# Kernel tuning notes

Measured on AMD Instinct MI355X. Metric: run time of the kernel, lower is better.

The kernel has to match this reference:

```python
import jax, jax.numpy as jnp
import numpy as np

WS = (4, 4, 4)  # window size
HEADS = 3
HEAD_DIM = 32

def _relative_indices():
    idx = np.array([[x, y, z] for x in range(WS[0]) for y in range(WS[1]) for z in range(WS[2])])
    rel = idx[None, :, :] - idx[:, None, :]  # [T, T, 3]
    rel = rel - rel.min()
    return rel  # values in [0, 2*ws-2]

_REL = _relative_indices()

def setup_inputs() -> dict:
    key = jax.random.key(0)
    k1, k2, k3, k4, k5 = jax.random.split(key, 5)
    dim = 96
    inner = HEADS * HEAD_DIM  # 96
    x = jax.random.normal(k1, (2, 64, 64, 64, dim), dtype=jnp.float32)
    w_qkv = jax.random.normal(k2, (dim, inner * 3), dtype=jnp.float32) * 0.02
    pos_embedding = jax.random.normal(k3, (7, 7, 7), dtype=jnp.float32)
    w_out = jax.random.normal(k4, (inner, dim), dtype=jnp.float32) * 0.02
    b_out = jax.random.normal(k5, (dim,), dtype=jnp.float32) * 0.02
    return {"x": x, "w_qkv": w_qkv, "pos_embedding": pos_embedding,
            "w_out": w_out, "b_out": b_out}

def reference(x, w_qkv, pos_embedding, w_out, b_out):
    b, H, W, D, C = x.shape
    wh, ww, wd = WS
    nwh, nww, nwd = H // wh, W // ww, D // wd
    nw = nwh * nww * nwd
    T = wh * ww * wd  # tokens per window
    scale = HEAD_DIM ** -0.5

    qkv = x @ w_qkv  # [b,H,W,D,3*inner]
    q, k, v = jnp.split(qkv, 3, axis=-1)

    def to_windows(t):
        # [b,H,W,D,h*d] -> [b, h, nw, T, d]
        t = t.reshape(b, nwh, wh, nww, ww, nwd, wd, HEADS, HEAD_DIM)
        t = t.transpose(0, 7, 1, 3, 5, 2, 4, 6, 8)
        return t.reshape(b, HEADS, nw, T, HEAD_DIM)

    q, k, v = map(to_windows, (q, k, v))

    dots = jnp.einsum('bhwid,bhwjd->bhwij', q, k) * scale  # [b,h,nw,T,T]
    bias = pos_embedding[_REL[:, :, 0], _REL[:, :, 1], _REL[:, :, 2]]  # [T,T]
    attn = jax.nn.softmax(dots + bias, axis=-1)
    out = jnp.einsum('bhwij,bhwjd->bhwid', attn, v)  # [b,h,nw,T,d]

    # back to [b,H,W,D,h*d]
    out = out.reshape(b, HEADS, nwh, nww, nwd, wh, ww, wd, HEAD_DIM)
    out = out.transpose(0, 2, 5, 3, 6, 4, 7, 1, 8)
    out = out.reshape(b, H, W, D, HEADS * HEAD_DIM)
    return out @ w_out + b_out
```

## Files before the change

kernel.cpp:

```cpp
#include <hip/hip_runtime.h>


typedef __attribute__((ext_vector_type(8))) short bv8;
typedef __attribute__((ext_vector_type(4))) float fv4;

__device__ __forceinline__ unsigned short f2bf(float f) {
    union { float f; unsigned u; } v; v.f = f;
    unsigned r = v.u + 0x7fffu + ((v.u >> 16) & 1u);
    return (unsigned short)(r >> 16);
}

__device__ __forceinline__ unsigned pack2(float lo, float hi) {
    return (unsigned)f2bf(lo) | ((unsigned)f2bf(hi) << 16);
}

__device__ __forceinline__ bv8 cvt8(const float* __restrict__ p) {
    float4 a = *(const float4*)p;
    float4 b = *(const float4*)(p + 4);
    bv8 r;
    r[0] = (short)f2bf(a.x); r[1] = (short)f2bf(a.y);
    r[2] = (short)f2bf(a.z); r[3] = (short)f2bf(a.w);
    r[4] = (short)f2bf(b.x); r[5] = (short)f2bf(b.y);
    r[6] = (short)f2bf(b.z); r[7] = (short)f2bf(b.w);
    return r;
}

#define REBUILD(dst, lo, hi)  do {                                              \
    unsigned w0 = (unsigned)__shfl((int)(lo)[0], lsrc0, 64);                    \
    unsigned w1 = (unsigned)__shfl((int)(lo)[1], lsrc0, 64);                    \
    unsigned w2 = (unsigned)__shfl((int)(lo)[0], lsrc1, 64);                    \
    unsigned w3 = (unsigned)__shfl((int)(lo)[1], lsrc1, 64);                    \
    unsigned v0 = (unsigned)__shfl((int)(hi)[0], lsrc0, 64);                    \
    unsigned v1 = (unsigned)__shfl((int)(hi)[1], lsrc0, 64);                    \
    unsigned v2 = (unsigned)__shfl((int)(hi)[0], lsrc1, 64);                    \
    unsigned v3 = (unsigned)__shfl((int)(hi)[1], lsrc1, 64);                    \
    unsigned u0 = selhi ? v0 : w0, u1 = selhi ? v1 : w1;                        \
    unsigned u2 = selhi ? v2 : w2, u3 = selhi ? v3 : w3;                        \
    bv8 p_;                                                                     \
    p_[0] = (short)(u0 & 0xffffu); p_[1] = (short)(u0 >> 16);                   \
    p_[2] = (short)(u1 & 0xffffu); p_[3] = (short)(u1 >> 16);                   \
    p_[4] = (short)(u2 & 0xffffu); p_[5] = (short)(u2 >> 16);                   \
    p_[6] = (short)(u3 & 0xffffu); p_[7] = (short)(u3 >> 16);                   \
    dst = p_;                                                                   \
} while (0)

__global__ void prep_kernel(const float* __restrict__ wqkv,
                            const float* __restrict__ wout,
                            const float* __restrict__ pos,
                            float* __restrict__ biasT,
                            unsigned short* __restrict__ wqT,
                            unsigned short* __restrict__ woT)
{
    int id = blockIdx.x * 256 + threadIdx.x;
    if (id < 27648) {
        int n = id / 96, k = id % 96;
        wqT[id] = f2bf(wqkv[k * 288 + n]);
    } else if (id < 36864) {
        int j = id - 27648;
        int n = j / 96, k = j % 96;
        woT[j] = f2bf(wout[k * 96 + n]);
    } else {
        int i = id - 36864;
        int kj = i >> 6, qi = i & 63;
        int dh = ((kj >> 4) & 3) - ((qi >> 4) & 3) + 3;
        int dw = ((kj >> 2) & 3) - ((qi >> 2) & 3) + 3;
        int dd = (kj & 3) - (qi & 3) + 3;
        biasT[kj * 64 + qi] = pos[(dh * 7 + dw) * 7 + dd] * 1.4426950408889634f;
    }
}

__global__ void __launch_bounds__(256, 4) winattn_kernel(
    const float* __restrict__ x,
    const float* __restrict__ b_out,
    const float* __restrict__ biasT,
    const unsigned short* __restrict__ wqT,
    const unsigned short* __restrict__ woT,
    float* __restrict__ out)
{
    __shared__ __align__(16) unsigned short ks[64 * 104];
    __shared__ __align__(16) unsigned short vts[96 * 72];

    const int tid = threadIdx.x;
    const int w = tid >> 6, lane = tid & 63;
    const int c = lane & 15, g = lane >> 4;
    const int widx = blockIdx.x, bb = blockIdx.y;
    const int bh = (widx >> 8) & 15, bw2 = (widx >> 4) & 15, bd = widx & 15;

    const int ST_W = 64 * 96, ST_H = 64 * 64 * 96;
    const int xbase = ((bb * 64 + bh * 4) * 64 + bw2 * 4) * 64 * 96 + bd * 4 * 96;
    const int i0 = w * 16;

    const int lsrc0 = (((2 * g) & 3) << 4) + c;
    const int lsrc1 = (((2 * g + 1) & 3) << 4) + c;
    const bool selhi = (g & 2) != 0;

    bv8 af[3];
    {
        int t = i0 + c;
        const float* tp = x + xbase + (t >> 4) * ST_H + ((t >> 2) & 3) * ST_W + (t & 3) * 96;
#pragma unroll
        for (int k = 0; k < 3; ++k)
            af[k] = cvt8(tp + k * 32 + g * 8);
    }

    const unsigned short* bsrc = wqT + c * 96 + g * 8;
    bv8 b0[3], bn[3];
#pragma unroll
    for (int k = 0; k < 3; ++k) b0[k] = *(const bv8*)(bsrc + k * 32);

    unsigned pkq[6][2];
#pragma unroll
    for (int nt = 0; nt < 18; ++nt) {
        if (nt < 17) {
#pragma unroll
            for (int k = 0; k < 3; ++k) bn[k] = *(const bv8*)(bsrc + (nt + 1) * 1536 + k * 32);
        }
        fv4 acc = {0.f, 0.f, 0.f, 0.f};
        if (nt < 6) {
#pragma unroll
            for (int k = 0; k < 3; ++k)
                acc = __builtin_amdgcn_mfma_f32_16x16x32_bf16(b0[k], af[k], acc, 0, 0, 0);
            pkq[nt][0] = pack2(acc[0], acc[1]);
            pkq[nt][1] = pack2(acc[2], acc[3]);
        } else if (nt < 12) {
#pragma unroll
            for (int k = 0; k < 3; ++k)
                acc = __builtin_amdgcn_mfma_f32_16x16x32_bf16(af[k], b0[k], acc, 0, 0, 0);
#pragma unroll
            for (int r = 0; r < 4; ++r)
                ks[(i0 + 4 * g + r) * 104 + (nt - 6) * 16 + c] = f2bf(acc[r]);
        } else {
#pragma unroll
            for (int k = 0; k < 3; ++k)
                acc = __builtin_amdgcn_mfma_f32_16x16x32_bf16(af[k], b0[k], acc, 0, 0, 0);
            int d = (nt - 12) * 16 + c;
            *(unsigned*)&vts[d * 72 + i0 + 4 * g]     = pack2(acc[0], acc[1]);
            *(unsigned*)&vts[d * 72 + i0 + 4 * g + 2] = pack2(acc[2], acc[3]);
        }
#pragma unroll
        for (int k = 0; k < 3; ++k) b0[k] = bn[k];
    }

    bv8 qf[3];
#pragma unroll
    for (int h = 0; h < 3; ++h)
        REBUILD(qf[h], pkq[2 * h], pkq[2 * h + 1]);

    float brow[4][4];
#pragma unroll
    for (int nt = 0; nt < 4; ++nt)
#pragma unroll
        for (int r = 0; r < 4; ++r)
            brow[nt][r] = biasT[(nt * 16 + 4 * g + r) * 64 + i0 + c];

    __syncthreads();

    const float scale2 = 0.17677669529663687f * 1.4426950408889634f;
    unsigned pko[6][2];

#pragma unroll
    for (int h = 0; h < 3; ++h) {
        bv8 kf[4];
#pragma unroll
        for (int nt = 0; nt < 4; ++nt)
            kf[nt] = *(const bv8*)&ks[(nt * 16 + c) * 104 + h * 32 + g * 8];
        float sv[4][4];
#pragma unroll
        for (int nt = 0; nt < 4; ++nt) {
            fv4 z = {0.f, 0.f, 0.f, 0.f};
            fv4 s = __builtin_amdgcn_mfma_f32_16x16x32_bf16(kf[nt], qf[h], z, 0, 0, 0);
#pragma unroll
            for (int r = 0; r < 4; ++r)
                sv[nt][r] = s[r] * scale2 + brow[nt][r];
        }
        float sm = 0.f;
#pragma unroll
        for (int nt = 0; nt < 4; ++nt)
#pragma unroll
            for (int r = 0; r < 4; ++r) {
                float e = exp2f(sv[nt][r]);
                sv[nt][r] = e;
                sm += e;
            }
        sm += __shfl_xor(sm, 16, 64);
        sm += __shfl_xor(sm, 32, 64);
        float inv = __builtin_amdgcn_rcpf(sm);

        unsigned pk[4][2];
#pragma unroll
        for (int nt = 0; nt < 4; ++nt) {
            pk[nt][0] = pack2(sv[nt][0], sv[nt][1]);
            pk[nt][1] = pack2(sv[nt][2], sv[nt][3]);
        }
        bv8 pf[2];
#pragma unroll
        for (int k2 = 0; k2 < 2; ++k2)
            REBUILD(pf[k2], pk[2 * k2], pk[2 * k2 + 1]);

#pragma unroll
        for (int dt = 0; dt < 2; ++dt) {
            fv4 oacc = {0.f, 0.f, 0.f, 0.f};
#pragma unroll
            for (int k2 = 0; k2 < 2; ++k2) {
                bv8 vf = *(const bv8*)&vts[(h * 32 + dt * 16 + c) * 72 + k2 * 32 + g * 8];
                oacc = __builtin_amdgcn_mfma_f32_16x16x32_bf16(vf, pf[k2], oacc, 0, 0, 0);
            }
            pko[2 * h + dt][0] = pack2(oacc[0] * inv, oacc[1] * inv);
            pko[2 * h + dt][1] = pack2(oacc[2] * inv, oacc[3] * inv);
        }
    }

    bv8 afo[3];
#pragma unroll
    for (int k = 0; k < 3; ++k)
        REBUILD(afo[k], pko[2 * k], pko[2 * k + 1]);

    const unsigned short* osrc = woT + c * 96 + g * 8;
    bv8 ob0[3], obn[3];
#pragma unroll
    for (int k = 0; k < 3; ++k) ob0[k] = *(const bv8*)(osrc + k * 32);

#pragma unroll
    for (int nt = 0; nt < 6; ++nt) {
        if (nt < 5) {
#pragma unroll
            for (int k = 0; k < 3; ++k) obn[k] = *(const bv8*)(osrc + (nt + 1) * 1536 + k * 32);
        }
        fv4 acc = {0.f, 0.f, 0.f, 0.f};
#pragma unroll
        for (int k = 0; k < 3; ++k)
            acc = __builtin_amdgcn_mfma_f32_16x16x32_bf16(afo[k], ob0[k], acc, 0, 0, 0);
        int cc = nt * 16 + c;
        float bo = b_out[cc];
#pragma unroll
        for (int r = 0; r < 4; ++r) {
            int t = i0 + 4 * g + r;
            out[xbase + (t >> 4) * ST_H + ((t >> 2) & 3) * ST_W + (t & 3) * 96 + cc] = acc[r] + bo;
        }
#pragma unroll
        for (int k = 0; k < 3; ++k) ob0[k] = obn[k];
    }
}

extern "C" void kernel_launch(void* const* d_in, const int* in_sizes, int n_in,
                              void* d_out, int out_size, void* d_ws, size_t ws_size,
                              hipStream_t stream)
{
    const float* x    = (const float*)d_in[0];
    const float* wqkv = (const float*)d_in[1];
    const float* pos  = (const float*)d_in[2];
    const float* wout = (const float*)d_in[3];
    const float* bout = (const float*)d_in[4];
    float* out = (float*)d_out;

    float* biasT = (float*)d_ws;
    unsigned short* wqT = (unsigned short*)((char*)d_ws + 16384);
    unsigned short* woT = (unsigned short*)((char*)d_ws + 16384 + 55296);

    prep_kernel<<<160, 256, 0, stream>>>(wqkv, wout, pos, biasT, wqT, woT);
    winattn_kernel<<<dim3(4096, 2), 256, 0, stream>>>(x, bout, biasT, wqT, woT, out);
}
```

Measured before the change: 206.9 us.

## Stage Q and attention output through per-wave LDS instead of register shuffles

Q and the per-head attention output are now written to a per-wave LDS scratch buffer and read back as MFMA fragments, replacing register-held packed values and the cross-lane REBUILD shuffles. The QKV and output projection loops are no longer unrolled, and the softmax normalization moves onto the probabilities before the PV product. The aim is to cut register pressure and shuffle overhead so more waves can stay resident. The cost is extra LDS traffic, a larger LDS footprint per block that may limit occupancy, and the loop overhead of the rolled loops.

```diff
diff --git a/kernel.cpp b/kernel.cpp
--- a/kernel.cpp
+++ b/kernel.cpp
@@ -77,6 +77,7 @@
     const unsigned short* __restrict__ woT,
     float* __restrict__ out)
 {
+    __shared__ __align__(16) unsigned short au[4 * 16 * 104];
     __shared__ __align__(16) unsigned short ks[64 * 104];
     __shared__ __align__(16) unsigned short vts[96 * 72];
 
@@ -89,6 +90,7 @@
     const int ST_W = 64 * 96, ST_H = 64 * 64 * 96;
     const int xbase = ((bb * 64 + bh * 4) * 64 + bw2 * 4) * 64 * 96 + bd * 4 * 96;
     const int i0 = w * 16;
+    unsigned short* auw = au + w * (16 * 104);
 
     const int lsrc0 = (((2 * g) & 3) << 4) + c;
     const int lsrc1 = (((2 * g + 1) & 3) << 4) + c;
@@ -108,43 +110,40 @@
 #pragma unroll
     for (int k = 0; k < 3; ++k) b0[k] = *(const bv8*)(bsrc + k * 32);
 
-    unsigned pkq[6][2];
-#pragma unroll
+#pragma unroll 1
     for (int nt = 0; nt < 18; ++nt) {
         if (nt < 17) {
 #pragma unroll
             for (int k = 0; k < 3; ++k) bn[k] = *(const bv8*)(bsrc + (nt + 1) * 1536 + k * 32);
         }
         fv4 acc = {0.f, 0.f, 0.f, 0.f};
+#pragma unroll
+        for (int k = 0; k < 3; ++k)
+            acc = __builtin_amdgcn_mfma_f32_16x16x32_bf16(af[k], b0[k], acc, 0, 0, 0);
         if (nt < 6) {
 #pragma unroll
-            for (int k = 0; k < 3; ++k)
-                acc = __builtin_amdgcn_mfma_f32_16x16x32_bf16(b0[k], af[k], acc, 0, 0, 0);
-            pkq[nt][0] = pack2(acc[0], acc[1]);
-            pkq[nt][1] = pack2(acc[2], acc[3]);
+            for (int r = 0; r < 4; ++r)
+                auw[(4 * g + r) * 104 + nt * 16 + c] = f2bf(acc[r]);
         } else if (nt < 12) {
-#pragma unroll
-            for (int k = 0; k < 3; ++k)
-                acc = __builtin_amdgcn_mfma_f32_16x16x32_bf16(af[k], b0[k], acc, 0, 0, 0);
 #pragma unroll
             for (int r = 0; r < 4; ++r)
                 ks[(i0 + 4 * g + r) * 104 + (nt - 6) * 16 + c] = f2bf(acc[r]);
         } else {
-#pragma unroll
-            for (int k = 0; k < 3; ++k)
-                acc = __builtin_amdgcn_mfma_f32_16x16x32_bf16(af[k], b0[k], acc, 0, 0, 0);
             int d = (nt - 12) * 16 + c;
             *(unsigned*)&vts[d * 72 + i0 + 4 * g]     = pack2(acc[0], acc[1]);
             *(unsigned*)&vts[d * 72 + i0 + 4 * g + 2] = pack2(acc[2], acc[3]);
         }
-#pragma unroll
-        for (int k = 0; k < 3; ++k) b0[k] = bn[k];
-    }
+        if (nt < 17) {
+#pragma unroll
+            for (int k = 0; k < 3; ++k) b0[k] = bn[k];
+        }
+    }
+    __syncthreads();
 
     bv8 qf[3];
 #pragma unroll
     for (int h = 0; h < 3; ++h)
-        REBUILD(qf[h], pkq[2 * h], pkq[2 * h + 1]);
+        qf[h] = *(const bv8*)&auw[c * 104 + h * 32 + g * 8];
 
     float brow[4][4];
 #pragma unroll
@@ -153,10 +152,7 @@
         for (int r = 0; r < 4; ++r)
             brow[nt][r] = biasT[(nt * 16 + 4 * g + r) * 64 + i0 + c];
 
-    __syncthreads();
-
     const float scale2 = 0.17677669529663687f * 1.4426950408889634f;
-    unsigned pko[6][2];
 
 #pragma unroll
     for (int h = 0; h < 3; ++h) {
@@ -189,8 +185,8 @@
         unsigned pk[4][2];
 #pragma unroll
         for (int nt = 0; nt < 4; ++nt) {
-            pk[nt][0] = pack2(sv[nt][0], sv[nt][1]);
-            pk[nt][1] = pack2(sv[nt][2], sv[nt][3]);
+            pk[nt][0] = pack2(sv[nt][0] * inv, sv[nt][1] * inv);
+            pk[nt][1] = pack2(sv[nt][2] * inv, sv[nt][3] * inv);
         }
         bv8 pf[2];
 #pragma unroll
@@ -203,24 +199,25 @@
 #pragma unroll
             for (int k2 = 0; k2 < 2; ++k2) {
                 bv8 vf = *(const bv8*)&vts[(h * 32 + dt * 16 + c) * 72 + k2 * 32 + g * 8];
-                oacc = __builtin_amdgcn_mfma_f32_16x16x32_bf16(vf, pf[k2], oacc, 0, 0, 0);
+                oacc = __builtin_amdgcn_mfma_f32_16x16x32_bf16(pf[k2], vf, oacc, 0, 0, 0);
             }
-            pko[2 * h + dt][0] = pack2(oacc[0] * inv, oacc[1] * inv);
-            pko[2 * h + dt][1] = pack2(oacc[2] * inv, oacc[3] * inv);
+#pragma unroll
+            for (int r = 0; r < 4; ++r)
+                auw[(4 * g + r) * 104 + h * 32 + dt * 16 + c] = f2bf(oacc[r]);
         }
     }
 
     bv8 afo[3];
 #pragma unroll
     for (int k = 0; k < 3; ++k)
-        REBUILD(afo[k], pko[2 * k], pko[2 * k + 1]);
+        afo[k] = *(const bv8*)&auw[c * 104 + k * 32 + g * 8];
 
     const unsigned short* osrc = woT + c * 96 + g * 8;
     bv8 ob0[3], obn[3];
 #pragma unroll
     for (int k = 0; k < 3; ++k) ob0[k] = *(const bv8*)(osrc + k * 32);
 
-#pragma unroll
+#pragma unroll 1
     for (int nt = 0; nt < 6; ++nt) {
         if (nt < 5) {
 #pragma unroll
@@ -237,8 +234,10 @@
             int t = i0 + 4 * g + r;
             out[xbase + (t >> 4) * ST_H + ((t >> 2) & 3) * ST_W + (t & 3) * 96 + cc] = acc[r] + bo;
         }
-#pragma unroll
-        for (int k = 0; k < 3; ++k) ob0[k] = obn[k];
+        if (nt < 5) {
+#pragma unroll
+            for (int k = 0; k < 3; ++k) ob0[k] = obn[k];
+        }
     }
 }
 
```

New measurement: 198.6 us. 4.0% less time.
